# Performance work log

Hardware: AMD Instinct MI355X
Metric: run time of the kernel (lower is better)

Reference implementation:

```python
import jax, jax.numpy as jnp
import numpy as np

TOKENS, HIDDEN, FFN = 4096, 4096, 14336
SCALE = 0.02  # keep activations in a sane range


def setup_inputs() -> dict:
    key = jax.random.key(0)
    k1, k2, k3, k4 = jax.random.split(key, 4)
    x = jax.random.normal(k1, (TOKENS, HIDDEN), dtype=jnp.float32)
    expert_w1 = jax.random.normal(k2, (FFN, HIDDEN), dtype=jnp.float32) * SCALE
    expert_v1 = jax.random.normal(k3, (FFN, HIDDEN), dtype=jnp.float32) * SCALE
    expert_w2 = jax.random.normal(k4, (FFN, HIDDEN), dtype=jnp.float32) * SCALE
    return {"x": x, "expert_w1": expert_w1, "expert_v1": expert_v1, "expert_w2": expert_w2}


def reference(x, expert_w1, expert_v1, expert_w2):
    # gate/up projections: [T, H] @ [H, F] -> [T, F]
    gate = jnp.einsum('th,fh->tf', x, expert_w1)
    up = jnp.einsum('th,fh->tf', x, expert_v1)
    inter = jax.nn.silu(gate) * up            # fused SwiGLU intermediate [T, F]
    down = jnp.einsum('tf,fh->th', inter, expert_w2)  # [T, H]
    return down
```

## Files before the change

kernel.cpp:

```cpp
#include <hip/hip_runtime.h>
#include <hip/hip_bf16.h>
#include <stdint.h>

#define TOKENS 4096
#define HIDDEN 4096
#define FFN    14336

typedef __attribute__((ext_vector_type(8))) short bf16x8;
typedef __attribute__((ext_vector_type(4))) float f32x4;
typedef __attribute__((ext_vector_type(8))) unsigned short u16x8;

typedef __attribute__((address_space(3))) void lds_void_t;
typedef const __attribute__((address_space(1))) void gbl_void_t;

static __device__ __forceinline__ unsigned short f2b(float f) {
  union { float f; unsigned int u; } v; v.f = f;
  unsigned int u = v.u;
  return (unsigned short)((u + 0x7FFFu + ((u >> 16) & 1u)) >> 16);
}

__global__ void cvt_kernel(const float* __restrict__ in, unsigned short* __restrict__ out, long n) {
  long idx = (long)blockIdx.x * blockDim.x + threadIdx.x;
  long stride = (long)gridDim.x * blockDim.x;
  for (long i = idx * 4; i < n; i += stride * 4) {
    const float4 v = *reinterpret_cast<const float4*>(in + i);
    ushort4 o;
    o.x = f2b(v.x); o.y = f2b(v.y); o.z = f2b(v.z); o.w = f2b(v.w);
    *reinterpret_cast<ushort4*>(out + i) = o;
  }
}

__global__ void transpose_cvt_kernel(const float* __restrict__ in, unsigned short* __restrict__ out) {
  __shared__ float tile[64][65];
  const int f0 = blockIdx.x * 64;
  const int h0 = blockIdx.y * 64;
  const int t = threadIdx.x;
  const int rcol = (t & 15) * 4;
  const int rrow = t >> 4;
#pragma unroll
  for (int it = 0; it < 4; ++it) {
    int r = rrow + it * 16;
    const float4 v = *reinterpret_cast<const float4*>(in + (long)(f0 + r) * HIDDEN + h0 + rcol);
    tile[r][rcol] = v.x; tile[r][rcol + 1] = v.y; tile[r][rcol + 2] = v.z; tile[r][rcol + 3] = v.w;
  }
  __syncthreads();
  const int wrow = t >> 2;
  const int wc = (t & 3) * 16;
  u16x8 lo, hi;
#pragma unroll
  for (int j = 0; j < 8; ++j) lo[j] = f2b(tile[wc + j][wrow]);
#pragma unroll
  for (int j = 0; j < 8; ++j) hi[j] = f2b(tile[wc + 8 + j][wrow]);
  u16x8* dst = reinterpret_cast<u16x8*>(out + (long)(h0 + wrow) * FFN + f0 + wc);
  dst[0] = lo; dst[1] = hi;
}

#define MFMA16(a, b, c) __builtin_amdgcn_mfma_f32_16x16x32_bf16((a), (b), (c), 0, 0, 0)
#define SBAR()  __builtin_amdgcn_s_barrier()
#define SCHED0() __builtin_amdgcn_sched_barrier(0)

__global__ __launch_bounds__(512, 2)
void gateup256_kernel(const unsigned short* __restrict__ X,
                      const unsigned short* __restrict__ W1,
                      const unsigned short* __restrict__ V1,
                      unsigned short* __restrict__ Inter) {
  __shared__ unsigned short sh[65536];
  const int tid = threadIdx.x, lane = tid & 63, wid = tid >> 6;
  const int wm = wid >> 2, wn = wid & 3;
  const int bm = blockIdx.x & 15;
  const int bn = blockIdx.x >> 4;
  const int sr = tid >> 3;
  const int scb = (((tid & 7) ^ (sr & 7)) << 4);
  const int l15 = lane & 15;
  const int cb0 = (((lane >> 4) * 16) ^ ((lane & 7) << 4));
  const int cb1 = ((64 + (lane >> 4) * 16) ^ ((lane & 7) << 4));

  const unsigned short* Ap = X  + (long)(bm * 256) * HIDDEN;
  const unsigned short* Wp = W1 + (long)(bn * 128) * HIDDEN;
  const unsigned short* Vp = V1 + (long)(bn * 128) * HIDDEN;

  f32x4 accg[8][2] = {};
  f32x4 accu[8][2] = {};

  auto STA = [&](int u, int buf, int t) {
    const unsigned short* src = Ap + (long)(u * 64 + sr) * HIDDEN + t * 64 + (scb >> 1);
    unsigned short* dst = sh + buf * 32768 + u * 4096 + tid * 8;
    __builtin_amdgcn_global_load_lds((gbl_void_t*)src, (lds_void_t*)dst, 16, 0, 0);
  };
  auto STW = [&](int u, int buf, int t) {
    const unsigned short* src = Wp + (long)(u * 64 + sr) * HIDDEN + t * 64 + (scb >> 1);
    unsigned short* dst = sh + buf * 32768 + 16384 + u * 4096 + tid * 8;
    __builtin_amdgcn_global_load_lds((gbl_void_t*)src, (lds_void_t*)dst, 16, 0, 0);
  };
  auto STV = [&](int u, int buf, int t) {
    const unsigned short* src = Vp + (long)(u * 64 + sr) * HIDDEN + t * 64 + (scb >> 1);
    unsigned short* dst = sh + buf * 32768 + 24576 + u * 4096 + tid * 8;
    __builtin_amdgcn_global_load_lds((gbl_void_t*)src, (lds_void_t*)dst, 16, 0, 0);
  };
  auto LDA8 = [&](bf16x8* a, int buf, int cb) {
    const char* base = (const char*)sh + buf * 65536 + wm * 16384 + l15 * 128 + cb;
#pragma unroll
    for (int m = 0; m < 8; ++m) a[m] = *(const bf16x8*)(base + m * 2048);
  };
  auto LDW2 = [&](bf16x8* w, int buf, int cb) {
    const char* base = (const char*)sh + buf * 65536 + 32768 + (wn * 32 + l15) * 128 + cb;
    w[0] = *(const bf16x8*)(base);
    w[1] = *(const bf16x8*)(base + 2048);
  };
  auto LDV2 = [&](bf16x8* v, int buf, int cb) {
    const char* base = (const char*)sh + buf * 65536 + 49152 + (wn * 32 + l15) * 128 + cb;
    v[0] = *(const bf16x8*)(base);
    v[1] = *(const bf16x8*)(base + 2048);
  };

  STA(0, 0, 0); STA(1, 0, 0); STA(2, 0, 0); STA(3, 0, 0);
  STW(0, 0, 0); STW(1, 0, 0); STV(0, 0, 0); STV(1, 0, 0);

  bf16x8 a[8], w[2], v[2];
  const int NT = HIDDEN / 64;
  for (int t = 0; t < NT; ++t) {
    const int cur = t & 1, nxt = cur ^ 1;
    const bool pre = (t + 1 < NT);
    if (pre) { STW(0, nxt, t + 1); STW(1, nxt, t + 1);
               STV(0, nxt, t + 1); STV(1, nxt, t + 1);
               asm volatile("s_waitcnt vmcnt(4)" ::: "memory"); }
    else     { asm volatile("s_waitcnt vmcnt(0)" ::: "memory"); }
    SBAR(); SCHED0();
    LDA8(a, cur, cb0); LDW2(w, cur, cb0);
    __builtin_amdgcn_s_setprio(1);
#pragma unroll
    for (int m = 0; m < 8; ++m) {
      accg[m][0] = MFMA16(a[m], w[0], accg[m][0]);
      accg[m][1] = MFMA16(a[m], w[1], accg[m][1]);
    }
    __builtin_amdgcn_s_setprio(0);
    SCHED0(); SBAR();
    LDV2(v, cur, cb0);
    if (pre) { STA(0, nxt, t + 1); STA(1, nxt, t + 1);
               STA(2, nxt, t + 1); STA(3, nxt, t + 1); }
    SCHED0(); SBAR();
    __builtin_amdgcn_s_setprio(1);
#pragma unroll
    for (int m = 0; m < 8; ++m) {
      accu[m][0] = MFMA16(a[m], v[0], accu[m][0]);
      accu[m][1] = MFMA16(a[m], v[1], accu[m][1]);
    }
    __builtin_amdgcn_s_setprio(0);
    SCHED0(); SBAR();
    LDA8(a, cur, cb1); LDW2(w, cur, cb1);
    SCHED0(); SBAR();
    __builtin_amdgcn_s_setprio(1);
#pragma unroll
    for (int m = 0; m < 8; ++m) {
      accg[m][0] = MFMA16(a[m], w[0], accg[m][0]);
      accg[m][1] = MFMA16(a[m], w[1], accg[m][1]);
    }
    __builtin_amdgcn_s_setprio(0);
    SCHED0(); SBAR();
    LDV2(v, cur, cb1);
    SCHED0(); SBAR();
    __builtin_amdgcn_s_setprio(1);
#pragma unroll
    for (int m = 0; m < 8; ++m) {
      accu[m][0] = MFMA16(a[m], v[0], accu[m][0]);
      accu[m][1] = MFMA16(a[m], v[1], accu[m][1]);
    }
    __builtin_amdgcn_s_setprio(0);
    SCHED0(); SBAR();
  }
  const int r0 = (lane >> 4) * 4;
#pragma unroll
  for (int m = 0; m < 8; ++m)
#pragma unroll
    for (int n = 0; n < 2; ++n)
#pragma unroll
      for (int r = 0; r < 4; ++r) {
        const float g = accg[m][n][r];
        const float u = accu[m][n][r];
        const float s = g / (1.0f + __expf(-g));
        const int row = bm * 256 + wm * 128 + m * 16 + r0 + r;
        const int col = bn * 128 + wn * 32 + n * 16 + l15;
        Inter[(long)row * FFN + col] = f2b(s * u);
      }
}

__global__ __launch_bounds__(512, 2)
void down256_kernel(const unsigned short* __restrict__ Inter,
                    const unsigned short* __restrict__ W2t,
                    float* __restrict__ Out) {
  __shared__ unsigned short sh[65536];
  const int tid = threadIdx.x, lane = tid & 63, wid = tid >> 6;
  const int wm = wid >> 2, wn = wid & 3;
  const int bm = blockIdx.x & 15;
  const int bn = blockIdx.x >> 4;
  const int sr = tid >> 3;
  const int scb = (((tid & 7) ^ (sr & 7)) << 4);
  const int l15 = lane & 15;
  const int cb0 = (((lane >> 4) * 16) ^ ((lane & 7) << 4));
  const int cb1 = ((64 + (lane >> 4) * 16) ^ ((lane & 7) << 4));

  const unsigned short* Ap = Inter + (long)(bm * 256) * FFN;
  const unsigned short* Bp = W2t + (long)(bn * 256) * FFN;

  f32x4 acc[8][4] = {};

  auto STAGE = [&](int kind, int h, int buf, int t) {
    const unsigned short* src = (kind ? Bp : Ap) + (long)(h * 128 + sr) * FFN + t * 64 + (scb >> 1);
    unsigned short* dst = sh + buf * 32768 + kind * 16384 + h * 8192 + tid * 8;
    __builtin_amdgcn_global_load_lds((gbl_void_t*)src, (lds_void_t*)dst, 16, 0, 0);
    __builtin_amdgcn_global_load_lds((gbl_void_t*)(src + 64L * FFN), (lds_void_t*)(dst + 4096), 16, 0, 0);
  };
  auto LDA8 = [&](bf16x8* a, int buf, int cb) {
    const char* base = (const char*)sh + buf * 65536 + wm * 16384 + l15 * 128 + cb;
#pragma unroll
    for (int m = 0; m < 8; ++m) a[m] = *(const bf16x8*)(base + m * 2048);
  };
  auto LDB2 = [&](bf16x8* b, int buf, int cb, int np) {
    const char* base = (const char*)sh + buf * 65536 + 32768 + (wn >> 1) * 16384 +
                       ((wn & 1) * 64 + l15) * 128 + cb;
    b[2 * np]     = *(const bf16x8*)(base + (2 * np) * 2048);
    b[2 * np + 1] = *(const bf16x8*)(base + (2 * np + 1) * 2048);
  };

  STAGE(0, 0, 0, 0); STAGE(0, 1, 0, 0); STAGE(1, 0, 0, 0); STAGE(1, 1, 0, 0);

  bf16x8 a[8], b[4];
  const int NT = FFN / 64;
  for (int t = 0; t < NT; ++t) {
    const int cur = t & 1, nxt = cur ^ 1;
    const bool pre = (t + 1 < NT);
    if (pre) { STAGE(1, 0, nxt, t + 1); STAGE(1, 1, nxt, t + 1);
               asm volatile("s_waitcnt vmcnt(4)" ::: "memory"); }
    else     { asm volatile("s_waitcnt vmcnt(0)" ::: "memory"); }
    SBAR(); SCHED0();
    LDA8(a, cur, cb0); LDB2(b, cur, cb0, 0);
    __builtin_amdgcn_s_setprio(1);
#pragma unroll
    for (int m = 0; m < 8; ++m) {
      acc[m][0] = MFMA16(a[m], b[0], acc[m][0]);
      acc[m][1] = MFMA16(a[m], b[1], acc[m][1]);
    }
    __builtin_amdgcn_s_setprio(0);
    SCHED0(); SBAR();
    LDB2(b, cur, cb0, 1);
    if (pre) { STAGE(0, 0, nxt, t + 1); STAGE(0, 1, nxt, t + 1); }
    SCHED0(); SBAR();
    __builtin_amdgcn_s_setprio(1);
#pragma unroll
    for (int m = 0; m < 8; ++m) {
      acc[m][2] = MFMA16(a[m], b[2], acc[m][2]);
      acc[m][3] = MFMA16(a[m], b[3], acc[m][3]);
    }
    __builtin_amdgcn_s_setprio(0);
    SCHED0(); SBAR();
    LDA8(a, cur, cb1); LDB2(b, cur, cb1, 0);
    SCHED0(); SBAR();
    __builtin_amdgcn_s_setprio(1);
#pragma unroll
    for (int m = 0; m < 8; ++m) {
      acc[m][0] = MFMA16(a[m], b[0], acc[m][0]);
      acc[m][1] = MFMA16(a[m], b[1], acc[m][1]);
    }
    __builtin_amdgcn_s_setprio(0);
    SCHED0(); SBAR();
    LDB2(b, cur, cb1, 1);
    SCHED0(); SBAR();
    __builtin_amdgcn_s_setprio(1);
#pragma unroll
    for (int m = 0; m < 8; ++m) {
      acc[m][2] = MFMA16(a[m], b[2], acc[m][2]);
      acc[m][3] = MFMA16(a[m], b[3], acc[m][3]);
    }
    __builtin_amdgcn_s_setprio(0);
    SCHED0(); SBAR();
  }
  const int r0 = (lane >> 4) * 4;
#pragma unroll
  for (int m = 0; m < 8; ++m)
#pragma unroll
    for (int n = 0; n < 4; ++n)
#pragma unroll
      for (int r = 0; r < 4; ++r) {
        const int row = bm * 256 + wm * 128 + m * 16 + r0 + r;
        const int col = bn * 256 + wn * 64 + n * 16 + l15;
        Out[(long)row * HIDDEN + col] = acc[m][n][r];
      }
}

__device__ __forceinline__ void stage_tile_128(const unsigned short* __restrict__ g, long ldk,
                                               unsigned short* lds, int wave, int lane) {
#pragma unroll
  for (int it = 0; it < 2; ++it) {
    const int row = (it * 4 + wave) * 16 + (lane >> 2);
    const int kcol = (lane & 3) * 8;
    const unsigned short* src = g + (long)row * ldk + kcol;
    unsigned short* dst = lds + row * 32 + kcol;
    __builtin_amdgcn_global_load_lds((gbl_void_t*)src, (lds_void_t*)dst, 16, 0, 0);
  }
}

__global__ __launch_bounds__(256, 2)
void down_nt_kernel(const unsigned short* __restrict__ Inter,
                    const float* __restrict__ W2,
                    float* __restrict__ Out) {
  __shared__ unsigned short As[128 * 32];
  __shared__ unsigned short Bs[128 * 32];
  const int t = threadIdx.x;
  const int lane = t & 63;
  const int wave = t >> 6;
  const int bm = blockIdx.x & 31;
  const int bn = blockIdx.x >> 5;
  const int wm = (wave >> 1) * 64;
  const int wn = (wave & 1) * 64;
  const unsigned short* gA = Inter + (long)(bm * 128) * FFN;

  f32x4 acc[4][4] = {};
  const int fr = lane & 15;
  const int kg = (lane >> 4) * 8;
  const int p = lane & 15;
  const int h0 = wave * 32 + (lane >> 4) * 8;
  const float* gB = W2 + bn * 128 + h0;

  for (int kt = 0; kt < FFN; kt += 32) {
    __syncthreads();
    stage_tile_128(gA + kt, FFN, As, wave, lane);
    const float* r0p = gB + (long)(kt + 2 * p) * HIDDEN;
    const float* r1p = r0p + HIDDEN;
    const float4 a0 = *reinterpret_cast<const float4*>(r0p);
    const float4 a1 = *reinterpret_cast<const float4*>(r0p + 4);
    const float4 b0 = *reinterpret_cast<const float4*>(r1p);
    const float4 b1 = *reinterpret_cast<const float4*>(r1p + 4);
    unsigned short lo[8], hi[8];
    lo[0] = f2b(a0.x); lo[1] = f2b(a0.y); lo[2] = f2b(a0.z); lo[3] = f2b(a0.w);
    lo[4] = f2b(a1.x); lo[5] = f2b(a1.y); lo[6] = f2b(a1.z); lo[7] = f2b(a1.w);
    hi[0] = f2b(b0.x); hi[1] = f2b(b0.y); hi[2] = f2b(b0.z); hi[3] = f2b(b0.w);
    hi[4] = f2b(b1.x); hi[5] = f2b(b1.y); hi[6] = f2b(b1.z); hi[7] = f2b(b1.w);
#pragma unroll
    for (int j = 0; j < 8; ++j) {
      const unsigned int pack = (unsigned int)lo[j] | ((unsigned int)hi[j] << 16);
      *reinterpret_cast<unsigned int*>(&Bs[(h0 + j) * 32 + 2 * p]) = pack;
    }
    __syncthreads();
    bf16x8 a[4], b[4];
#pragma unroll
    for (int m = 0; m < 4; ++m)
      a[m] = *reinterpret_cast<const bf16x8*>(&As[(wm + m * 16 + fr) * 32 + kg]);
#pragma unroll
    for (int n = 0; n < 4; ++n)
      b[n] = *reinterpret_cast<const bf16x8*>(&Bs[(wn + n * 16 + fr) * 32 + kg]);
#pragma unroll
    for (int m = 0; m < 4; ++m)
#pragma unroll
      for (int n = 0; n < 4; ++n)
        acc[m][n] = MFMA16(a[m], b[n], acc[m][n]);
  }
  const int r0 = (lane >> 4) * 4;
#pragma unroll
  for (int m = 0; m < 4; ++m)
#pragma unroll
    for (int n = 0; n < 4; ++n)
#pragma unroll
      for (int r = 0; r < 4; ++r) {
        const int row = bm * 128 + wm + m * 16 + r0 + r;
        const int col = bn * 128 + wn + n * 16 + fr;
        Out[(long)row * HIDDEN + col] = acc[m][n][r];
      }
}

extern "C" void kernel_launch(void* const* d_in, const int* in_sizes, int n_in,
                              void* d_out, int out_size, void* d_ws, size_t ws_size,
                              hipStream_t stream) {
  const float* x  = (const float*)d_in[0];
  const float* w1 = (const float*)d_in[1];
  const float* v1 = (const float*)d_in[2];
  const float* w2 = (const float*)d_in[3];
  float* out = (float*)d_out;

  const size_t REQ_SMALL = 385875968UL;
  const size_t REQ_FULL  = 503316480UL;
  if (ws_size < REQ_SMALL) return;
  const bool full = (ws_size >= REQ_FULL);
  char* ws = (char*)d_ws;
  unsigned short* xb     = (unsigned short*)(ws);
  unsigned short* w1b    = (unsigned short*)(ws + 33554432L);
  unsigned short* v1b    = (unsigned short*)(ws + 150994944L);
  unsigned short* interb = (unsigned short*)(ws + 268435456L);
  unsigned short* w2tb   = (unsigned short*)(ws + 385875968L);

  hipLaunchKernelGGL(cvt_kernel, dim3(2048), dim3(256), 0, stream, x,  xb,  (long)TOKENS * HIDDEN);
  hipLaunchKernelGGL(cvt_kernel, dim3(2048), dim3(256), 0, stream, w1, w1b, (long)FFN * HIDDEN);
  hipLaunchKernelGGL(cvt_kernel, dim3(2048), dim3(256), 0, stream, v1, v1b, (long)FFN * HIDDEN);
  if (full)
    hipLaunchKernelGGL(transpose_cvt_kernel, dim3(FFN / 64, HIDDEN / 64), dim3(256), 0, stream, w2, w2tb);
  hipLaunchKernelGGL(gateup256_kernel, dim3((TOKENS / 256) * (FFN / 128)), dim3(512), 0, stream,
                     xb, w1b, v1b, interb);
  if (full)
    hipLaunchKernelGGL(down256_kernel, dim3((TOKENS / 256) * (HIDDEN / 256)), dim3(512), 0, stream,
                       interb, w2tb, out);
  else
    hipLaunchKernelGGL(down_nt_kernel, dim3((TOKENS / 128) * (HIDDEN / 128)), dim3(256), 0, stream,
                       interb, w2, out);
}
```

Baseline: 1.449 ms.

## Split gate/up across waves and combine SwiGLU via LDS exchange

```diff
diff --git a/kernel.cpp b/kernel.cpp
--- a/kernel.cpp
+++ b/kernel.cpp
@@ -17,6 +17,10 @@
   union { float f; unsigned int u; } v; v.f = f;
   unsigned int u = v.u;
   return (unsigned short)((u + 0x7FFFu + ((u >> 16) & 1u)) >> 16);
+}
+static __device__ __forceinline__ float b2f(unsigned short b) {
+  union { unsigned int u; float f; } v; v.u = ((unsigned int)b) << 16;
+  return v.f;
 }
 
 __global__ void cvt_kernel(const float* __restrict__ in, unsigned short* __restrict__ out, long n) {
@@ -60,10 +64,10 @@
 #define SCHED0() __builtin_amdgcn_sched_barrier(0)
 
 __global__ __launch_bounds__(512, 2)
-void gateup256_kernel(const unsigned short* __restrict__ X,
-                      const unsigned short* __restrict__ W1,
-                      const unsigned short* __restrict__ V1,
-                      unsigned short* __restrict__ Inter) {
+void gateup256b_kernel(const unsigned short* __restrict__ X,
+                       const unsigned short* __restrict__ W1,
+                       const unsigned short* __restrict__ V1,
+                       unsigned short* __restrict__ Inter) {
   __shared__ unsigned short sh[65536];
   const int tid = threadIdx.x, lane = tid & 63, wid = tid >> 6;
   const int wm = wid >> 2, wn = wid & 3;
@@ -79,109 +83,113 @@
   const unsigned short* Wp = W1 + (long)(bn * 128) * HIDDEN;
   const unsigned short* Vp = V1 + (long)(bn * 128) * HIDDEN;
 
-  f32x4 accg[8][2] = {};
-  f32x4 accu[8][2] = {};
-
-  auto STA = [&](int u, int buf, int t) {
-    const unsigned short* src = Ap + (long)(u * 64 + sr) * HIDDEN + t * 64 + (scb >> 1);
-    unsigned short* dst = sh + buf * 32768 + u * 4096 + tid * 8;
+  f32x4 acc[8][4] = {};
+
+  auto STAGE = [&](int kind, int h, int buf, int t) {
+    const unsigned short* src;
+    if (kind == 0) src = Ap + (long)(h * 128 + sr) * HIDDEN + t * 64 + (scb >> 1);
+    else           src = (h ? Vp : Wp) + (long)sr * HIDDEN + t * 64 + (scb >> 1);
+    unsigned short* dst = sh + buf * 32768 + kind * 16384 + h * 8192 + tid * 8;
     __builtin_amdgcn_global_load_lds((gbl_void_t*)src, (lds_void_t*)dst, 16, 0, 0);
-  };
-  auto STW = [&](int u, int buf, int t) {
-    const unsigned short* src = Wp + (long)(u * 64 + sr) * HIDDEN + t * 64 + (scb >> 1);
-    unsigned short* dst = sh + buf * 32768 + 16384 + u * 4096 + tid * 8;
-    __builtin_amdgcn_global_load_lds((gbl_void_t*)src, (lds_void_t*)dst, 16, 0, 0);
-  };
-  auto STV = [&](int u, int buf, int t) {
-    const unsigned short* src = Vp + (long)(u * 64 + sr) * HIDDEN + t * 64 + (scb >> 1);
-    unsigned short* dst = sh + buf * 32768 + 24576 + u * 4096 + tid * 8;
-    __builtin_amdgcn_global_load_lds((gbl_void_t*)src, (lds_void_t*)dst, 16, 0, 0);
+    __builtin_amdgcn_global_load_lds((gbl_void_t*)(src + 64L * HIDDEN), (lds_void_t*)(dst + 4096), 16, 0, 0);
   };
   auto LDA8 = [&](bf16x8* a, int buf, int cb) {
     const char* base = (const char*)sh + buf * 65536 + wm * 16384 + l15 * 128 + cb;
 #pragma unroll
     for (int m = 0; m < 8; ++m) a[m] = *(const bf16x8*)(base + m * 2048);
   };
-  auto LDW2 = [&](bf16x8* w, int buf, int cb) {
-    const char* base = (const char*)sh + buf * 65536 + 32768 + (wn * 32 + l15) * 128 + cb;
-    w[0] = *(const bf16x8*)(base);
-    w[1] = *(const bf16x8*)(base + 2048);
-  };
-  auto LDV2 = [&](bf16x8* v, int buf, int cb) {
-    const char* base = (const char*)sh + buf * 65536 + 49152 + (wn * 32 + l15) * 128 + cb;
-    v[0] = *(const bf16x8*)(base);
-    v[1] = *(const bf16x8*)(base + 2048);
-  };
-
-  STA(0, 0, 0); STA(1, 0, 0); STA(2, 0, 0); STA(3, 0, 0);
-  STW(0, 0, 0); STW(1, 0, 0); STV(0, 0, 0); STV(1, 0, 0);
-
-  bf16x8 a[8], w[2], v[2];
+  auto LDB2 = [&](bf16x8* b, int buf, int cb, int np) {
+    const char* base = (const char*)sh + buf * 65536 + 32768 + (wn >> 1) * 16384 +
+                       ((wn & 1) * 64 + l15) * 128 + cb;
+    b[2 * np]     = *(const bf16x8*)(base + (2 * np) * 2048);
+    b[2 * np + 1] = *(const bf16x8*)(base + (2 * np + 1) * 2048);
+  };
+
+  STAGE(0, 0, 0, 0); STAGE(0, 1, 0, 0); STAGE(1, 0, 0, 0); STAGE(1, 1, 0, 0);
+
+  bf16x8 a[8], b[4];
   const int NT = HIDDEN / 64;
   for (int t = 0; t < NT; ++t) {
     const int cur = t & 1, nxt = cur ^ 1;
     const bool pre = (t + 1 < NT);
-    if (pre) { STW(0, nxt, t + 1); STW(1, nxt, t + 1);
-               STV(0, nxt, t + 1); STV(1, nxt, t + 1);
+    if (pre) { STAGE(1, 0, nxt, t + 1); STAGE(1, 1, nxt, t + 1);
                asm volatile("s_waitcnt vmcnt(4)" ::: "memory"); }
     else     { asm volatile("s_waitcnt vmcnt(0)" ::: "memory"); }
     SBAR(); SCHED0();
-    LDA8(a, cur, cb0); LDW2(w, cur, cb0);
-    __builtin_amdgcn_s_setprio(1);
-#pragma unroll
-    for (int m = 0; m < 8; ++m) {
-      accg[m][0] = MFMA16(a[m], w[0], accg[m][0]);
-      accg[m][1] = MFMA16(a[m], w[1], accg[m][1]);
-    }
-    __builtin_amdgcn_s_setprio(0);
-    SCHED0(); SBAR();
-    LDV2(v, cur, cb0);
-    if (pre) { STA(0, nxt, t + 1); STA(1, nxt, t + 1);
-               STA(2, nxt, t + 1); STA(3, nxt, t + 1); }
-    SCHED0(); SBAR();
-    __builtin_amdgcn_s_setprio(1);
-#pragma unroll
-    for (int m = 0; m < 8; ++m) {
-      accu[m][0] = MFMA16(a[m], v[0], accu[m][0]);
-      accu[m][1] = MFMA16(a[m], v[1], accu[m][1]);
-    }
-    __builtin_amdgcn_s_setprio(0);
-    SCHED0(); SBAR();
-    LDA8(a, cur, cb1); LDW2(w, cur, cb1);
-    SCHED0(); SBAR();
-    __builtin_amdgcn_s_setprio(1);
-#pragma unroll
-    for (int m = 0; m < 8; ++m) {
-      accg[m][0] = MFMA16(a[m], w[0], accg[m][0]);
-      accg[m][1] = MFMA16(a[m], w[1], accg[m][1]);
-    }
-    __builtin_amdgcn_s_setprio(0);
-    SCHED0(); SBAR();
-    LDV2(v, cur, cb1);
-    SCHED0(); SBAR();
-    __builtin_amdgcn_s_setprio(1);
-#pragma unroll
-    for (int m = 0; m < 8; ++m) {
-      accu[m][0] = MFMA16(a[m], v[0], accu[m][0]);
-      accu[m][1] = MFMA16(a[m], v[1], accu[m][1]);
-    }
-    __builtin_amdgcn_s_setprio(0);
-    SCHED0(); SBAR();
-  }
-  const int r0 = (lane >> 4) * 4;
-#pragma unroll
-  for (int m = 0; m < 8; ++m)
-#pragma unroll
-    for (int n = 0; n < 2; ++n)
-#pragma unroll
-      for (int r = 0; r < 4; ++r) {
-        const float g = accg[m][n][r];
-        const float u = accu[m][n][r];
-        const float s = g / (1.0f + __expf(-g));
-        const int row = bm * 256 + wm * 128 + m * 16 + r0 + r;
-        const int col = bn * 128 + wn * 32 + n * 16 + l15;
-        Inter[(long)row * FFN + col] = f2b(s * u);
+    LDA8(a, cur, cb0); LDB2(b, cur, cb0, 0);
+    __builtin_amdgcn_s_setprio(1);
+#pragma unroll
+    for (int m = 0; m < 8; ++m) {
+      acc[m][0] = MFMA16(a[m], b[0], acc[m][0]);
+      acc[m][1] = MFMA16(a[m], b[1], acc[m][1]);
+    }
+    __builtin_amdgcn_s_setprio(0);
+    SCHED0(); SBAR();
+    LDB2(b, cur, cb0, 1);
+    if (pre) { STAGE(0, 0, nxt, t + 1); STAGE(0, 1, nxt, t + 1); }
+    SCHED0(); SBAR();
+    __builtin_amdgcn_s_setprio(1);
+#pragma unroll
+    for (int m = 0; m < 8; ++m) {
+      acc[m][2] = MFMA16(a[m], b[2], acc[m][2]);
+      acc[m][3] = MFMA16(a[m], b[3], acc[m][3]);
+    }
+    __builtin_amdgcn_s_setprio(0);
+    SCHED0(); SBAR();
+    LDA8(a, cur, cb1); LDB2(b, cur, cb1, 0);
+    SCHED0(); SBAR();
+    __builtin_amdgcn_s_setprio(1);
+#pragma unroll
+    for (int m = 0; m < 8; ++m) {
+      acc[m][0] = MFMA16(a[m], b[0], acc[m][0]);
+      acc[m][1] = MFMA16(a[m], b[1], acc[m][1]);
+    }
+    __builtin_amdgcn_s_setprio(0);
+    SCHED0(); SBAR();
+    LDB2(b, cur, cb1, 1);
+    SCHED0(); SBAR();
+    __builtin_amdgcn_s_setprio(1);
+#pragma unroll
+    for (int m = 0; m < 8; ++m) {
+      acc[m][2] = MFMA16(a[m], b[2], acc[m][2]);
+      acc[m][3] = MFMA16(a[m], b[3], acc[m][3]);
+    }
+    __builtin_amdgcn_s_setprio(0);
+    SCHED0(); SBAR();
+  }
+  __syncthreads();
+  if (wn >= 2) {
+#pragma unroll
+    for (int m = 0; m < 8; ++m)
+#pragma unroll
+      for (int n = 0; n < 4; ++n) {
+        ushort4 p;
+        p.x = f2b(acc[m][n][0]); p.y = f2b(acc[m][n][1]);
+        p.z = f2b(acc[m][n][2]); p.w = f2b(acc[m][n][3]);
+        const int idx = ((((wm * 2 + (wn & 1)) * 8 + m) * 4 + n) * 64 + lane) * 4;
+        *reinterpret_cast<ushort4*>(&sh[idx]) = p;
       }
+  }
+  __syncthreads();
+  if (wn < 2) {
+    const int r0 = (lane >> 4) * 4;
+#pragma unroll
+    for (int m = 0; m < 8; ++m)
+#pragma unroll
+      for (int n = 0; n < 4; ++n) {
+        const int idx = ((((wm * 2 + wn) * 8 + m) * 4 + n) * 64 + lane) * 4;
+        const ushort4 p = *reinterpret_cast<const ushort4*>(&sh[idx]);
+        const float uu[4] = { b2f(p.x), b2f(p.y), b2f(p.z), b2f(p.w) };
+        const int row = bm * 256 + wm * 128 + m * 16 + r0;
+        const int col = bn * 128 + wn * 64 + n * 16 + l15;
+#pragma unroll
+        for (int r = 0; r < 4; ++r) {
+          const float g = acc[m][n][r];
+          const float s = g / (1.0f + __expf(-g));
+          Inter[(long)(row + r) * FFN + col] = f2b(s * uu[r]);
+        }
+      }
+  }
 }
 
 __global__ __launch_bounds__(512, 2)
@@ -392,7 +400,7 @@
   hipLaunchKernelGGL(cvt_kernel, dim3(2048), dim3(256), 0, stream, v1, v1b, (long)FFN * HIDDEN);
   if (full)
     hipLaunchKernelGGL(transpose_cvt_kernel, dim3(FFN / 64, HIDDEN / 64), dim3(256), 0, stream, w2, w2tb);
-  hipLaunchKernelGGL(gateup256_kernel, dim3((TOKENS / 256) * (FFN / 128)), dim3(512), 0, stream,
+  hipLaunchKernelGGL(gateup256b_kernel, dim3((TOKENS / 256) * (FFN / 128)), dim3(512), 0, stream,
                      xb, w1b, v1b, interb);
   if (full)
     hipLaunchKernelGGL(down256_kernel, dim3((TOKENS / 256) * (HIDDEN / 256)), dim3(512), 0, stream,
```

New measurement: 1.475 ms. No clear change (+1.7%).

## Halve barriers per k-step and swizzle workgroups across XCDs in both GEMMs

Applied to the files above, without the earlier changes.

```diff
diff --git a/kernel.cpp b/kernel.cpp
--- a/kernel.cpp
+++ b/kernel.cpp
@@ -59,6 +59,10 @@
 #define SBAR()  __builtin_amdgcn_s_barrier()
 #define SCHED0() __builtin_amdgcn_sched_barrier(0)
 
+static __device__ __forceinline__ int xcd_chunk(int bid, int nwg) {
+  return (bid & 7) * (nwg >> 3) + (bid >> 3);
+}
+
 __global__ __launch_bounds__(512, 2)
 void gateup256_kernel(const unsigned short* __restrict__ X,
                       const unsigned short* __restrict__ W1,
@@ -67,8 +71,9 @@
   __shared__ unsigned short sh[65536];
   const int tid = threadIdx.x, lane = tid & 63, wid = tid >> 6;
   const int wm = wid >> 2, wn = wid & 3;
-  const int bm = blockIdx.x & 15;
-  const int bn = blockIdx.x >> 4;
+  const int swz = xcd_chunk(blockIdx.x, (TOKENS / 256) * (FFN / 128));
+  const int bm = swz & 15;
+  const int bn = swz >> 4;
   const int sr = tid >> 3;
   const int scb = (((tid & 7) ^ (sr & 7)) << 4);
   const int l15 = lane & 15;
@@ -134,11 +139,13 @@
       accg[m][1] = MFMA16(a[m], w[1], accg[m][1]);
     }
     __builtin_amdgcn_s_setprio(0);
-    SCHED0(); SBAR();
-    LDV2(v, cur, cb0);
+    SCHED0();
+    asm volatile("s_waitcnt lgkmcnt(0)" ::: "memory");
+    SBAR();
     if (pre) { STA(0, nxt, t + 1); STA(1, nxt, t + 1);
                STA(2, nxt, t + 1); STA(3, nxt, t + 1); }
-    SCHED0(); SBAR();
+    SCHED0();
+    LDV2(v, cur, cb0);
     __builtin_amdgcn_s_setprio(1);
 #pragma unroll
     for (int m = 0; m < 8; ++m) {
@@ -146,9 +153,11 @@
       accu[m][1] = MFMA16(a[m], v[1], accu[m][1]);
     }
     __builtin_amdgcn_s_setprio(0);
-    SCHED0(); SBAR();
+    SCHED0();
+    asm volatile("s_waitcnt lgkmcnt(0)" ::: "memory");
+    SBAR();
+    SCHED0();
     LDA8(a, cur, cb1); LDW2(w, cur, cb1);
-    SCHED0(); SBAR();
     __builtin_amdgcn_s_setprio(1);
 #pragma unroll
     for (int m = 0; m < 8; ++m) {
@@ -156,9 +165,11 @@
       accg[m][1] = MFMA16(a[m], w[1], accg[m][1]);
     }
     __builtin_amdgcn_s_setprio(0);
-    SCHED0(); SBAR();
+    SCHED0();
+    asm volatile("s_waitcnt lgkmcnt(0)" ::: "memory");
+    SBAR();
+    SCHED0();
     LDV2(v, cur, cb1);
-    SCHED0(); SBAR();
     __builtin_amdgcn_s_setprio(1);
 #pragma unroll
     for (int m = 0; m < 8; ++m) {
@@ -166,7 +177,9 @@
       accu[m][1] = MFMA16(a[m], v[1], accu[m][1]);
     }
     __builtin_amdgcn_s_setprio(0);
-    SCHED0(); SBAR();
+    SCHED0();
+    asm volatile("s_waitcnt lgkmcnt(0)" ::: "memory");
+    SBAR();
   }
   const int r0 = (lane >> 4) * 4;
 #pragma unroll
@@ -191,8 +204,9 @@
   __shared__ unsigned short sh[65536];
   const int tid = threadIdx.x, lane = tid & 63, wid = tid >> 6;
   const int wm = wid >> 2, wn = wid & 3;
-  const int bm = blockIdx.x & 15;
-  const int bn = blockIdx.x >> 4;
+  const int swz = xcd_chunk(blockIdx.x, (TOKENS / 256) * (HIDDEN / 256));
+  const int bm = swz & 15;
+  const int bn = swz >> 4;
   const int sr = tid >> 3;
   const int scb = (((tid & 7) ^ (sr & 7)) << 4);
   const int l15 = lane & 15;
@@ -241,10 +255,12 @@
       acc[m][1] = MFMA16(a[m], b[1], acc[m][1]);
     }
     __builtin_amdgcn_s_setprio(0);
-    SCHED0(); SBAR();
+    SCHED0();
+    asm volatile("s_waitcnt lgkmcnt(0)" ::: "memory");
+    SBAR();
+    if (pre) { STAGE(0, 0, nxt, t + 1); STAGE(0, 1, nxt, t + 1); }
+    SCHED0();
     LDB2(b, cur, cb0, 1);
-    if (pre) { STAGE(0, 0, nxt, t + 1); STAGE(0, 1, nxt, t + 1); }
-    SCHED0(); SBAR();
     __builtin_amdgcn_s_setprio(1);
 #pragma unroll
     for (int m = 0; m < 8; ++m) {
@@ -252,9 +268,11 @@
       acc[m][3] = MFMA16(a[m], b[3], acc[m][3]);
     }
     __builtin_amdgcn_s_setprio(0);
-    SCHED0(); SBAR();
+    SCHED0();
+    asm volatile("s_waitcnt lgkmcnt(0)" ::: "memory");
+    SBAR();
+    SCHED0();
     LDA8(a, cur, cb1); LDB2(b, cur, cb1, 0);
-    SCHED0(); SBAR();
     __builtin_amdgcn_s_setprio(1);
 #pragma unroll
     for (int m = 0; m < 8; ++m) {
@@ -262,9 +280,11 @@
       acc[m][1] = MFMA16(a[m], b[1], acc[m][1]);
     }
     __builtin_amdgcn_s_setprio(0);
-    SCHED0(); SBAR();
+    SCHED0();
+    asm volatile("s_waitcnt lgkmcnt(0)" ::: "memory");
+    SBAR();
+    SCHED0();
     LDB2(b, cur, cb1, 1);
-    SCHED0(); SBAR();
     __builtin_amdgcn_s_setprio(1);
 #pragma unroll
     for (int m = 0; m < 8; ++m) {
@@ -272,7 +292,9 @@
       acc[m][3] = MFMA16(a[m], b[3], acc[m][3]);
     }
     __builtin_amdgcn_s_setprio(0);
-    SCHED0(); SBAR();
+    SCHED0();
+    asm volatile("s_waitcnt lgkmcnt(0)" ::: "memory");
+    SBAR();
   }
   const int r0 = (lane >> 4) * 4;
 #pragma unroll
```

New measurement: 1.432 ms. About the same (-1.2%).
